# Kernel optimization log

Measured on AMD Instinct MI355X. Metric: run time of the kernel, lower is better.

## Reference

```python
import jax, jax.numpy as jnp
import numpy as np

KERNEL_SIZE = 5
SIGMA = 1.0
DARK_KS = 15


def _gaussian_kernel():
    x = jnp.arange(KERNEL_SIZE, dtype=jnp.float32) - KERNEL_SIZE // 2
    phi = jnp.exp(-0.5 * x * x / (SIGMA ** 2))
    phi = phi / (phi.sum() + 0.001)
    k2d = jnp.outer(phi, phi)                       # [5,5]
    return jnp.tile(k2d[None, None], (3, 1, 1, 1))  # [3,1,5,5] OIHW depthwise


def _tanh01(v):
    return jnp.tanh(v) * 0.5 + 0.5


def setup_inputs() -> dict:
    key = jax.random.key(0)
    k1, k2, k3 = jax.random.split(key, 3)
    # keep x strictly positive so x**param has well-defined gradients
    x = jax.random.uniform(k1, (16, 3, 512, 512), dtype=jnp.float32, minval=0.01, maxval=1.0)
    output1 = jax.random.normal(k2, (16, 7), dtype=jnp.float32)
    output2 = jax.random.normal(k3, (16, 4), dtype=jnp.float32)
    return {"x": x, "output1": output1, "output2": output2}


def reference(x, output1, output2):
    N, C, H, W = x.shape

    # ---- parameter squashing (clip_range + softmax weights) ----
    o1 = jnp.concatenate([
        _tanh01(output1[:, 0:1]) * 0.25 + 1.0,   # gamma param in [1, 1.25]
        _tanh01(output1[:, 1:2]) * 0.9 + 0.1,    # contrast alpha (dead branch)
        _tanh01(output1[:, 2:3]) * 2.0,          # sharpen lamda in [0, 2]
        _tanh01(output1[:, 3:4]),                # dehaze w in [0, 1]
        _tanh01(output1[:, 4:7]) * 0.1 + 0.95,   # WB gains in [0.95, 1.05]
    ], axis=1)
    o2 = jax.nn.softmax(_tanh01(output2), axis=1)  # [N,4] branch weights

    param = o1[:, 0][:, None, None, None]
    lamda = o1[:, 2][:, None, None, None]
    w = o1[:, 3][:, None, None, None]
    wb_params = o1[:, 4:7][:, :, None, None]

    # ---- WB ----
    x1 = jnp.clip(x * wb_params, 0.0, 1.0)

    # ---- GAMMA ----
    x2 = jnp.clip(x ** param + 0.001, 0.0, 1.0)

    # ---- SHARPEN (depthwise 5x5 gaussian blur, unsharp mask) ----
    gk = _gaussian_kernel()
    blur = jax.lax.conv_general_dilated(
        x, gk, window_strides=(1, 1), padding=((2, 2), (2, 2)),
        feature_group_count=3,
        dimension_numbers=("NCHW", "OIHW", "NCHW"))
    blur = jnp.clip(blur, 0.0, 1.0)
    x4 = jnp.clip(x + lamda * (x - blur), 0.0, 1.0)

    # ---- DEHAZE ----
    minc = jnp.min(x, axis=1, keepdims=True)  # [N,1,H,W]
    # avg_pool2d k=15 s=1 p=7 with count_include_pad=True -> sum window / 225
    dark = jax.lax.reduce_window(
        minc, 0.0, jax.lax.add, (1, 1, DARK_KS, DARK_KS), (1, 1, 1, 1),
        padding=[(0, 0), (0, 0), (DARK_KS // 2, DARK_KS // 2), (DARK_KS // 2, DARK_KS // 2)]
    ) / float(DARK_KS * DARK_KS)
    top_k = int(H * W * 0.05)
    flat_dark = dark.reshape(N, -1)
    _, top_idx = jax.lax.top_k(flat_dark, top_k)            # [N, top_k]
    flat_img = x.reshape(N, C, -1)
    sel = jnp.take_along_axis(flat_img, top_idx[:, None, :], axis=2)  # [N,C,top_k]
    A = sel.mean(axis=2)[:, :, None, None]                  # atmospheric light
    trans = 1.0 - w * dark
    trans = jnp.where(trans > 0.1, trans, jnp.float32(0.1))
    x5 = jnp.clip((x - A) / (trans + 0.001) + A, 0.0, 1.0)

    # ---- weighted combination (contrast branch is computed but unused upstream) ----
    w0 = o2[:, 0][:, None, None, None]
    w1 = o2[:, 1][:, None, None, None]
    w2 = o2[:, 2][:, None, None, None]
    w3 = o2[:, 3][:, None, None, None]
    x_sum = x + 0.1 * (w0 * x1 + w1 * x2 + w2 * x4 + w3 * x5)
    x_sum = x_sum / (jnp.sum(o2, axis=1)[:, None, None, None] + 0.001)

    # ---- per-sample per-channel min-max normalization ----
    min_vals = jnp.min(x_sum, axis=(2, 3), keepdims=True)
    max_vals = jnp.max(x_sum, axis=(2, 3), keepdims=True)
    return (x_sum - min_vals) / (max_vals - min_vals + 1e-07)
```

## Files before the change

### kernel.cpp

```cpp
#include <hip/hip_runtime.h>
#include <math.h>

#define NS   16
#define HH   512
#define WW   512
#define HW   (HH*WW)
#define TOPK 13107
#define NBIN 1024

#define O_O1   0
#define O_O2   112
#define O_DEN  176
#define O_KN   304
#define O_MMP  512
#define O_PART 25088
#define O_DARK 33280


#define G0 0.054466787f
#define G1 0.244103071f
#define G2 0.402457854f

__device__ __forceinline__ float tanh01(float v) { return tanhf(v)*0.5f + 0.5f; }
__device__ __forceinline__ float clamp01(float v) { return fminf(fmaxf(v, 0.0f), 1.0f); }
__device__ __forceinline__ int dark_bin(float v) {
  int b = (int)(v * (float)NBIN);
  return b > (NBIN-1) ? (NBIN-1) : (b < 0 ? 0 : b);
}

__device__ __forceinline__ float4 ld_halo(const float* __restrict__ xc, int i,
                                          int h0, int w0, bool interior) {
  int rr = i / 18, q = i - rr*18;
  int gh = h0 - 2 + rr, gw = w0 - 4 + 4*q;
  if (interior) return *(const float4*)&xc[(size_t)gh*WW + gw];
  float4 v; v.x = 0.f; v.y = 0.f; v.z = 0.f; v.w = 0.f;
  if (gh >= 0 && gh < HH && gw >= 0 && gw < WW)
    v = *(const float4*)&xc[(size_t)gh*WW + gw];
  return v;
}

__global__ void __launch_bounds__(512)
k_dark(const float* __restrict__ x, float* __restrict__ wsf, unsigned* __restrict__ hist,
       const float* __restrict__ o1, const float* __restrict__ o2) {
  __shared__ __align__(16) float sm[6240 + 78*64];
  float* minc = sm;
  unsigned* lh = (unsigned*)sm;
  float* hsum = sm + 6240;
  int tid = threadIdx.x;
  int swz = (blockIdx.x & 7) * 128 + (blockIdx.x >> 3);
  int n = swz >> 6, rem = swz & 63;
  int w0 = (rem & 7) * 64, h0 = (rem >> 3) * 64;
  const float* xb = x + (size_t)n*3*HW;

  if (rem == 0 && tid == 0) {
    wsf[O_O1+n*7+0] = tanh01(o1[n*7+0])*0.25f + 1.0f;
    wsf[O_O1+n*7+1] = tanh01(o1[n*7+1])*0.9f  + 0.1f;
    wsf[O_O1+n*7+2] = tanh01(o1[n*7+2])*2.0f;
    wsf[O_O1+n*7+3] = tanh01(o1[n*7+3]);
    wsf[O_O1+n*7+4] = tanh01(o1[n*7+4])*0.1f + 0.95f;
    wsf[O_O1+n*7+5] = tanh01(o1[n*7+5])*0.1f + 0.95f;
    wsf[O_O1+n*7+6] = tanh01(o1[n*7+6])*0.1f + 0.95f;
    float q0 = expf(tanh01(o2[n*4+0]));
    float q1 = expf(tanh01(o2[n*4+1]));
    float q2 = expf(tanh01(o2[n*4+2]));
    float q3 = expf(tanh01(o2[n*4+3]));
    float s = q0+q1+q2+q3;
    q0 /= s; q1 /= s; q2 /= s; q3 /= s;
    wsf[O_O2+n*4+0]=q0; wsf[O_O2+n*4+1]=q1; wsf[O_O2+n*4+2]=q2; wsf[O_O2+n*4+3]=q3;
    wsf[O_DEN+n] = (q0+q1+q2+q3) + 0.001f;
  }

  bool interior = (w0 >= 8) && (w0 + 72 <= WW) && (h0 >= 7) && (h0 + 71 <= HH);
  if (interior) {
    for (int i = tid; i < 78*20; i += 512) {
      int r = i / 20, q = i - r*20;
      size_t o = (size_t)(h0 - 7 + r)*WW + (w0 - 8 + 4*q);
      float4 a = *(const float4*)&xb[o];
      float4 b = *(const float4*)&xb[HW + o];
      float4 c = *(const float4*)&xb[2*HW + o];
      float4 v;
      v.x = fminf(fminf(a.x,b.x),c.x); v.y = fminf(fminf(a.y,b.y),c.y);
      v.z = fminf(fminf(a.z,b.z),c.z); v.w = fminf(fminf(a.w,b.w),c.w);
      *(float4*)&minc[r*80 + 4*q] = v;
    }
  } else {
    for (int i = tid; i < 78*20; i += 512) {
      int r = i / 20, q = i - r*20;
      int hm = h0 - 7 + r, wc = w0 - 8 + 4*q;
      float4 v; v.x = 0.f; v.y = 0.f; v.z = 0.f; v.w = 0.f;
      if (hm >= 0 && hm < HH && wc >= 0 && wc < WW) {
        size_t o = (size_t)hm*WW + wc;
        float4 a = *(const float4*)&xb[o];
        float4 b = *(const float4*)&xb[HW + o];
        float4 c = *(const float4*)&xb[2*HW + o];
        v.x = fminf(fminf(a.x,b.x),c.x); v.y = fminf(fminf(a.y,b.y),c.y);
        v.z = fminf(fminf(a.z,b.z),c.z); v.w = fminf(fminf(a.w,b.w),c.w);
      }
      *(float4*)&minc[r*80 + 4*q] = v;
    }
  }
  __syncthreads();
  for (int i = tid; i < 78*16; i += 512) {
    int r = i >> 4, c4 = (i & 15) * 4;
    const float4* mr = (const float4*)&minc[r*80];
    int qb = c4 >> 2;
    float m[20];
    #pragma unroll
    for (int t = 0; t < 5; ++t) {
      float4 v = mr[qb + t];
      m[4*t] = v.x; m[4*t+1] = v.y; m[4*t+2] = v.z; m[4*t+3] = v.w;
    }
    float s = 0.f;
    #pragma unroll
    for (int j = 1; j <= 15; ++j) s += m[j];
    float4 o;
    o.x = s; s += m[16] - m[1];
    o.y = s; s += m[17] - m[2];
    o.z = s; s += m[18] - m[3];
    o.w = s;
    *(float4*)&hsum[r*64 + c4] = o;
  }
  __syncthreads();
  {
    uint4 z4; z4.x = 0u; z4.y = 0u; z4.z = 0u; z4.w = 0u;
    for (int i = tid; i < NBIN; i += 512) ((uint4*)lh)[i] = z4;
  }
  __syncthreads();
  {
    int c = tid & 63, ty = tid >> 6, r0 = ty * 8;
    int rep = tid & 3;
    float s = 0.f;
    #pragma unroll
    for (int j = 0; j < 15; ++j) s += hsum[(r0 + j)*64 + c];
    float* dk = wsf + O_DARK + (size_t)n*HW;
    int prevb = -1; unsigned cnt = 0;
    #pragma unroll
    for (int i = 0; i < 8; ++i) {
      int r = r0 + i;
      float v = s * (1.0f/225.0f);
      dk[(size_t)(h0 + r)*WW + w0 + c] = v;
      int b = dark_bin(v);
      if (b == prevb) { cnt++; }
      else {
        if (cnt) atomicAdd(&lh[(prevb << 2) | rep], cnt);
        prevb = b; cnt = 1u;
      }
      if (i < 7) s += hsum[(r + 15)*64 + c] - hsum[r*64 + c];
    }
    atomicAdd(&lh[(prevb << 2) | rep], cnt);
  }
  __syncthreads();
  unsigned* gh = hist + n*NBIN;
  for (int b = tid; b < NBIN; b += 512) {
    unsigned v = lh[4*b] + lh[4*b+1] + lh[4*b+2] + lh[4*b+3];
    if (v) atomicAdd(&gh[b], v);
  }
}

__global__ void __launch_bounds__(256)
k_asum(const float* __restrict__ x, float* __restrict__ wsf,
       const unsigned* __restrict__ hist, unsigned* __restrict__ wsu) {
  __shared__ __align__(16) unsigned lh[NBIN];
  __shared__ unsigned spp[256];
  __shared__ unsigned wtot[4];
  __shared__ int sh_bsel;
  __shared__ unsigned sh_kn;
  __shared__ float bl[4][7];
  int tid = threadIdx.x;
  int lane = tid & 63, wave = tid >> 6;
  int swz = (blockIdx.x & 7) * 64 + (blockIdx.x >> 3);
  int n = swz >> 5, chunk = swz & 31;
  {
    uint4 v = ((const uint4*)(hist + n*NBIN))[tid];
    *(uint4*)&lh[tid*4] = v;
    spp[tid] = v.x + v.y + v.z + v.w;
  }
  __syncthreads();
  unsigned sv = spp[tid];
  #pragma unroll
  for (int off = 1; off < 64; off <<= 1) {
    unsigned u = __shfl_down(sv, off);
    if (lane + off < 64) sv += u;
  }
  if (lane == 0) wtot[wave] = sv;
  __syncthreads();
  unsigned above = 0;
  #pragma unroll
  for (int w2 = 1; w2 < 4; ++w2) above += (wave + w2 < 4) ? wtot[wave + w2] : 0u;
  unsigned S = sv + above;
  unsigned Snext = S - spp[tid];
  if (S >= (unsigned)TOPK && Snext < (unsigned)TOPK) {
    unsigned cum = Snext;
    int bsel = tid*4;
    for (int b = tid*4 + 3; b >= tid*4; --b) {
      if (cum + lh[b] >= (unsigned)TOPK) { bsel = b; break; }
      cum += lh[b];
    }
    sh_bsel = bsel;
    sh_kn = (unsigned)TOPK - cum;
  }
  __syncthreads();
  int bsel = sh_bsel;
  if (tid == 0 && chunk == 0) wsu[O_KN + n] = sh_kn;
  const float4* db = (const float4*)(wsf + O_DARK + (size_t)n*HW) + (size_t)chunk*2048;
  const float4* x0 = (const float4*)(x + (size_t)n*3*HW) + (size_t)chunk*2048;
  const float4* x1 = x0 + HW/4;
  const float4* x2 = x0 + HW/2;
  float s0=0,s1=0,s2=0,e0=0,e1=0,e2=0,ec=0;
  #pragma unroll
  for (int k = 0; k < 8; ++k) {
    int idx = k*256 + tid;
    float4 d = db[idx];
    int bbx = dark_bin(d.x), bby = dark_bin(d.y);
    int bbz = dark_bin(d.z), bbw = dark_bin(d.w);
    int bmax = bbx > bby ? bbx : bby;
    bmax = bbz > bmax ? bbz : bmax;
    bmax = bbw > bmax ? bbw : bmax;
    if (bmax >= bsel) {
      float4 a = x0[idx], b = x1[idx], c = x2[idx];
      #define ACC(BB, AX, BX, CX) { \
        bool gt = (BB > bsel), eq = (BB == bsel); \
        s0 += gt ? AX : 0.f; s1 += gt ? BX : 0.f; s2 += gt ? CX : 0.f; \
        e0 += eq ? AX : 0.f; e1 += eq ? BX : 0.f; e2 += eq ? CX : 0.f; \
        ec += eq ? 1.f : 0.f; }
      ACC(bbx, a.x, b.x, c.x) ACC(bby, a.y, b.y, c.y)
      ACC(bbz, a.z, b.z, c.z) ACC(bbw, a.w, b.w, c.w)
      #undef ACC
    }
  }
  #pragma unroll
  for (int off = 32; off; off >>= 1) {
    s0 += __shfl_down(s0, off); s1 += __shfl_down(s1, off); s2 += __shfl_down(s2, off);
    e0 += __shfl_down(e0, off); e1 += __shfl_down(e1, off); e2 += __shfl_down(e2, off);
    ec += __shfl_down(ec, off);
  }
  if (lane == 0) {
    bl[wave][0]=s0; bl[wave][1]=s1; bl[wave][2]=s2;
    bl[wave][3]=e0; bl[wave][4]=e1; bl[wave][5]=e2; bl[wave][6]=ec;
  }
  __syncthreads();
  if (tid < 7) wsf[O_PART + (size_t)swz*8 + tid] =
      bl[0][tid] + bl[1][tid] + bl[2][tid] + bl[3][tid];
}

__global__ void __launch_bounds__(256)
k_main(const float* __restrict__ x, float* __restrict__ wsf,
       const unsigned* __restrict__ wsu, float* __restrict__ out) {
  __shared__ __align__(16) float xs[36*72];
  __shared__ __align__(16) float hb[36*68];
  __shared__ float rmn[4], rmx[4];
  __shared__ float shA[3];
  int tid = threadIdx.x;
  int swz = (blockIdx.x & 7) * 256 + (blockIdx.x >> 3);
  int n = swz >> 7, bxy = swz & 127;
  int w0 = (bxy & 7) * 64, h0 = (bxy >> 3) * 32;
  int r2 = tid >> 4, c4 = (tid & 15) * 4;
  int wave = tid >> 6, lane = tid & 63;
  const float* dkp = wsf + O_DARK + (size_t)n*HW + (size_t)(h0 + 2*r2)*WW + w0 + c4;
  float4 dk0 = *(const float4*)dkp;
  float4 dk1 = *(const float4*)(dkp + WW);
  float param = wsf[O_O1 + n*7 + 0];
  float lamda = wsf[O_O1 + n*7 + 2];
  float wpar  = wsf[O_O1 + n*7 + 3];
  float wbc[3];
  wbc[0] = wsf[O_O1 + n*7 + 4];
  wbc[1] = wsf[O_O1 + n*7 + 5];
  wbc[2] = wsf[O_O1 + n*7 + 6];
  float q0 = wsf[O_O2 + n*4 + 0], q1 = wsf[O_O2 + n*4 + 1];
  float q2 = wsf[O_O2 + n*4 + 2], q3 = wsf[O_O2 + n*4 + 3];
  float rden = 1.0f / wsf[O_DEN + n];
  bool interior = (w0 >= 4) && (w0 + 68 <= WW) && (h0 >= 2) && (h0 + 34 <= HH);
  if (tid < 64) {
    float s0=0,s1=0,s2=0,e0=0,e1=0,e2=0,ec=0;
    if (tid < 32) {
      const float* p = wsf + O_PART + (size_t)(n*32 + tid)*8;
      s0=p[0]; s1=p[1]; s2=p[2]; e0=p[3]; e1=p[4]; e2=p[5]; ec=p[6];
    }
    #pragma unroll
    for (int off = 32; off; off >>= 1) {
      s0 += __shfl_down(s0, off); s1 += __shfl_down(s1, off); s2 += __shfl_down(s2, off);
      e0 += __shfl_down(e0, off); e1 += __shfl_down(e1, off); e2 += __shfl_down(e2, off);
      ec += __shfl_down(ec, off);
    }
    if (tid == 0) {
      float kn = (float)wsu[O_KN + n];
      float ce = fmaxf(ec, 1.0f);
      shA[0] = (s0 + kn * (e0 / ce)) * (1.0f/(float)TOPK);
      shA[1] = (s1 + kn * (e1 / ce)) * (1.0f/(float)TOPK);
      shA[2] = (s2 + kn * (e2 / ce)) * (1.0f/(float)TOPK);
    }
  }

  float4 pf0, pf1, pf2;
  #define LOADCH(cc) do { \
    const float* xc = x + (size_t)(n*3 + (cc))*HW; \
    pf0 = ld_halo(xc, tid,       h0, w0, interior); \
    pf1 = ld_halo(xc, tid + 256, h0, w0, interior); \
    if (tid < 136) pf2 = ld_halo(xc, tid + 512, h0, w0, interior); \
  } while (0)
  #define STORECH() do { \
    { int rr = tid/18, q = tid - rr*18; *(float4*)&xs[rr*72 + 4*q] = pf0; } \
    { int i2 = tid + 256; int rr = i2/18, q = i2 - rr*18; *(float4*)&xs[rr*72 + 4*q] = pf1; } \
    if (tid < 136) { int i2 = tid + 512; int rr = i2/18, q = i2 - rr*18; *(float4*)&xs[rr*72 + 4*q] = pf2; } \
  } while (0)

  LOADCH(0);
  STORECH();
  __syncthreads();

  for (int c = 0; c < 3; ++c) {
    int z = n*3 + c;
    for (int i = tid; i < 576; i += 256) {
      int rr = i >> 4, cc4 = (i & 15) * 4;
      const float4* xr = (const float4*)&xs[rr*72];
      int qb = cc4 >> 2;
      float4 A4 = xr[qb], B4 = xr[qb+1], C4 = xr[qb+2];
      float m2=A4.z, m3=A4.w, m4=B4.x, m5=B4.y, m6=B4.z, m7=B4.w, m8=C4.x, m9=C4.y;
      float4 o;
      o.x = G0*(m2+m6) + G1*(m3+m5) + G2*m4;
      o.y = G0*(m3+m7) + G1*(m4+m6) + G2*m5;
      o.z = G0*(m4+m8) + G1*(m5+m7) + G2*m6;
      o.w = G0*(m5+m9) + G1*(m6+m8) + G2*m7;
      *(float4*)&hb[rr*68 + cc4] = o;
    }
    if (c < 2) LOADCH(c + 1);
    __syncthreads();
    float wb = wbc[c];
    float A  = shA[c];
    float4 xv0 = *(const float4*)&xs[(2*r2+2)*72 + c4 + 4];
    float4 xv1 = *(const float4*)&xs[(2*r2+3)*72 + c4 + 4];
    float4 b0 = *(const float4*)&hb[(2*r2+0)*68 + c4];
    float4 b1 = *(const float4*)&hb[(2*r2+1)*68 + c4];
    float4 b2 = *(const float4*)&hb[(2*r2+2)*68 + c4];
    float4 b3 = *(const float4*)&hb[(2*r2+3)*68 + c4];
    float4 b4 = *(const float4*)&hb[(2*r2+4)*68 + c4];
    float4 b5 = *(const float4*)&hb[(2*r2+5)*68 + c4];
    float4 os0, os1;
    float mnv = 3.4e38f, mxv = -3.4e38f;
    #define PIX(OX, XV, B0, B1, B2, B3, B4, DK) { \
      float blur = clamp01(G0*(B0+B4) + G1*(B1+B3) + G2*B2); \
      float x4v = clamp01(XV + lamda*(XV - blur)); \
      float x1v = clamp01(XV * wb); \
      float x2v = clamp01(__expf(param*__logf(XV)) + 0.001f); \
      float tr = 1.0f - wpar*DK; tr = tr > 0.1f ? tr : 0.1f; \
      float x5v = clamp01((XV - A) * __builtin_amdgcn_rcpf(tr + 0.001f) + A); \
      OX = (XV + 0.1f*(q0*x1v + q1*x2v + q2*x4v + q3*x5v)) * rden; \
      mnv = fminf(mnv, OX); mxv = fmaxf(mxv, OX); }
    PIX(os0.x, xv0.x, b0.x, b1.x, b2.x, b3.x, b4.x, dk0.x)
    PIX(os0.y, xv0.y, b0.y, b1.y, b2.y, b3.y, b4.y, dk0.y)
    PIX(os0.z, xv0.z, b0.z, b1.z, b2.z, b3.z, b4.z, dk0.z)
    PIX(os0.w, xv0.w, b0.w, b1.w, b2.w, b3.w, b4.w, dk0.w)
    PIX(os1.x, xv1.x, b1.x, b2.x, b3.x, b4.x, b5.x, dk1.x)
    PIX(os1.y, xv1.y, b1.y, b2.y, b3.y, b4.y, b5.y, dk1.y)
    PIX(os1.z, xv1.z, b1.z, b2.z, b3.z, b4.z, b5.z, dk1.z)
    PIX(os1.w, xv1.w, b1.w, b2.w, b3.w, b4.w, b5.w, dk1.w)
    #undef PIX
    float* op = out + (size_t)z*HW + (size_t)(h0 + 2*r2)*WW + w0 + c4;
    *(float4*)op = os0;
    *(float4*)(op + WW) = os1;
    #pragma unroll
    for (int off = 32; off; off >>= 1) {
      mnv = fminf(mnv, __shfl_down(mnv, off));
      mxv = fmaxf(mxv, __shfl_down(mxv, off));
    }
    if (lane == 0) { rmn[wave] = mnv; rmx[wave] = mxv; }
    __syncthreads();
    if (tid == 0) {
      mnv = fminf(fminf(rmn[0], rmn[1]), fminf(rmn[2], rmn[3]));
      mxv = fmaxf(fmaxf(rmx[0], rmx[1]), fmaxf(rmx[2], rmx[3]));
      wsf[O_MMP + z*512 + bxy]       = mnv;
      wsf[O_MMP + z*512 + 256 + bxy] = mxv;
    }
    if (c < 2) {
      STORECH();
      __syncthreads();
    }
  }
  #undef LOADCH
  #undef STORECH
}

__global__ void __launch_bounds__(256)
k_norm(float* __restrict__ out, const float* __restrict__ wsf) {
  int tid = threadIdx.x;
  int bid = (blockIdx.x & 7) * 192 + (blockIdx.x >> 3);
  int nc = bid >> 5;
  int sub = bid & 31;
  int l = tid & 63;
  const float* pm = wsf + O_MMP + (size_t)nc*512;
  float mn = fminf(pm[l], pm[64 + l]);
  float mx = fmaxf(pm[256 + l], pm[320 + l]);
  #pragma unroll
  for (int off = 32; off; off >>= 1) {
    mn = fminf(mn, __shfl_down(mn, off));
    mx = fmaxf(mx, __shfl_down(mx, off));
  }
  mn = __shfl(mn, 0);
  mx = __shfl(mx, 0);
  float sc = 1.0f / (mx - mn + 1e-7f);
  float4* o4 = (float4*)out + (size_t)nc*65536 + (size_t)sub*2048;
  #pragma unroll
  for (int k = 0; k < 8; ++k) {
    float4 v = o4[k*256 + tid];
    v.x = (v.x - mn) * sc; v.y = (v.y - mn) * sc;
    v.z = (v.z - mn) * sc; v.w = (v.w - mn) * sc;
    o4[k*256 + tid] = v;
  }
}

extern "C" void kernel_launch(void* const* d_in, const int* in_sizes, int n_in,
                              void* d_out, int out_size, void* d_ws, size_t ws_size,
                              hipStream_t stream) {
  const float* x  = (const float*)d_in[0];
  const float* o1 = (const float*)d_in[1];
  const float* o2 = (const float*)d_in[2];
  float* out = (float*)d_out;
  float* wsf = (float*)d_ws;
  unsigned* wsu = (unsigned*)d_ws;
  unsigned* hist = (unsigned*)(out + (size_t)16*HW);

  hipMemsetAsync(hist, 0, (size_t)NS*NBIN*sizeof(unsigned), stream);
  k_dark<<<dim3(1024), dim3(512), 0, stream>>>(x, wsf, hist, o1, o2);
  k_asum<<<dim3(512), dim3(256), 0, stream>>>(x, wsf, hist, wsu);
  k_main<<<dim3(2048), dim3(256), 0, stream>>>(x, wsf, wsu, out);
  k_norm<<<dim3(1536), dim3(256), 0, stream>>>(out, wsf);
}
```

Baseline: 154.3 us.

## Fuse horizontal and vertical blur passes in registers, dropping shared blur buffer

Replaces the two-phase separable blur, which wrote horizontal results to a shared buffer and synchronized before the vertical pass, with per-thread computation. Each thread computes the six horizontal rows it needs and accumulates the vertical taps directly in registers. This removes the hb shared array and one __syncthreads per channel, and pads the xs row stride from 72 to 76 floats, likely to reduce LDS bank conflicts. In exchange each thread recomputes horizontal rows that neighbours also compute, adding redundant ALU work and LDS reads.

```diff
diff --git a/kernel.cpp b/kernel.cpp
--- a/kernel.cpp
+++ b/kernel.cpp
@@ -246,8 +246,7 @@
 __global__ void __launch_bounds__(256)
 k_main(const float* __restrict__ x, float* __restrict__ wsf,
        const unsigned* __restrict__ wsu, float* __restrict__ out) {
-  __shared__ __align__(16) float xs[36*72];
-  __shared__ __align__(16) float hb[36*68];
+  __shared__ __align__(16) float xs[36*76];
   __shared__ float rmn[4], rmx[4];
   __shared__ float shA[3];
   int tid = threadIdx.x;
@@ -299,46 +298,46 @@
     if (tid < 136) pf2 = ld_halo(xc, tid + 512, h0, w0, interior); \
   } while (0)
   #define STORECH() do { \
-    { int rr = tid/18, q = tid - rr*18; *(float4*)&xs[rr*72 + 4*q] = pf0; } \
-    { int i2 = tid + 256; int rr = i2/18, q = i2 - rr*18; *(float4*)&xs[rr*72 + 4*q] = pf1; } \
-    if (tid < 136) { int i2 = tid + 512; int rr = i2/18, q = i2 - rr*18; *(float4*)&xs[rr*72 + 4*q] = pf2; } \
+    { int rr = tid/18, q = tid - rr*18; *(float4*)&xs[rr*76 + 4*q] = pf0; } \
+    { int i2 = tid + 256; int rr = i2/18, q = i2 - rr*18; *(float4*)&xs[rr*76 + 4*q] = pf1; } \
+    if (tid < 136) { int i2 = tid + 512; int rr = i2/18, q = i2 - rr*18; *(float4*)&xs[rr*76 + 4*q] = pf2; } \
   } while (0)
 
   LOADCH(0);
   STORECH();
   __syncthreads();
 
+  int qb = c4 >> 2;
   for (int c = 0; c < 3; ++c) {
     int z = n*3 + c;
-    for (int i = tid; i < 576; i += 256) {
-      int rr = i >> 4, cc4 = (i & 15) * 4;
-      const float4* xr = (const float4*)&xs[rr*72];
-      int qb = cc4 >> 2;
+    if (c < 2) LOADCH(c + 1);
+    float4 acc0, acc1;
+    acc0.x = acc0.y = acc0.z = acc0.w = 0.f;
+    acc1.x = acc1.y = acc1.z = acc1.w = 0.f;
+    const float cA[6] = {G0, G1, G2, G1, G0, 0.f};
+    const float cB[6] = {0.f, G0, G1, G2, G1, G0};
+    #pragma unroll
+    for (int k = 0; k < 6; ++k) {
+      const float4* xr = (const float4*)&xs[(2*r2 + k)*76];
       float4 A4 = xr[qb], B4 = xr[qb+1], C4 = xr[qb+2];
       float m2=A4.z, m3=A4.w, m4=B4.x, m5=B4.y, m6=B4.z, m7=B4.w, m8=C4.x, m9=C4.y;
-      float4 o;
-      o.x = G0*(m2+m6) + G1*(m3+m5) + G2*m4;
-      o.y = G0*(m3+m7) + G1*(m4+m6) + G2*m5;
-      o.z = G0*(m4+m8) + G1*(m5+m7) + G2*m6;
-      o.w = G0*(m5+m9) + G1*(m6+m8) + G2*m7;
-      *(float4*)&hb[rr*68 + cc4] = o;
-    }
-    if (c < 2) LOADCH(c + 1);
-    __syncthreads();
+      float4 h;
+      h.x = G0*(m2+m6) + G1*(m3+m5) + G2*m4;
+      h.y = G0*(m3+m7) + G1*(m4+m6) + G2*m5;
+      h.z = G0*(m4+m8) + G1*(m5+m7) + G2*m6;
+      h.w = G0*(m5+m9) + G1*(m6+m8) + G2*m7;
+      float wa = cA[k], wb2 = cB[k];
+      acc0.x += wa*h.x; acc0.y += wa*h.y; acc0.z += wa*h.z; acc0.w += wa*h.w;
+      acc1.x += wb2*h.x; acc1.y += wb2*h.y; acc1.z += wb2*h.z; acc1.w += wb2*h.w;
+    }
     float wb = wbc[c];
     float A  = shA[c];
-    float4 xv0 = *(const float4*)&xs[(2*r2+2)*72 + c4 + 4];
-    float4 xv1 = *(const float4*)&xs[(2*r2+3)*72 + c4 + 4];
-    float4 b0 = *(const float4*)&hb[(2*r2+0)*68 + c4];
-    float4 b1 = *(const float4*)&hb[(2*r2+1)*68 + c4];
-    float4 b2 = *(const float4*)&hb[(2*r2+2)*68 + c4];
-    float4 b3 = *(const float4*)&hb[(2*r2+3)*68 + c4];
-    float4 b4 = *(const float4*)&hb[(2*r2+4)*68 + c4];
-    float4 b5 = *(const float4*)&hb[(2*r2+5)*68 + c4];
+    float4 xv0 = *(const float4*)&xs[(2*r2+2)*76 + c4 + 4];
+    float4 xv1 = *(const float4*)&xs[(2*r2+3)*76 + c4 + 4];
     float4 os0, os1;
     float mnv = 3.4e38f, mxv = -3.4e38f;
-    #define PIX(OX, XV, B0, B1, B2, B3, B4, DK) { \
-      float blur = clamp01(G0*(B0+B4) + G1*(B1+B3) + G2*B2); \
+    #define PIX(OX, XV, BL, DK) { \
+      float blur = clamp01(BL); \
       float x4v = clamp01(XV + lamda*(XV - blur)); \
       float x1v = clamp01(XV * wb); \
       float x2v = clamp01(__expf(param*__logf(XV)) + 0.001f); \
@@ -346,14 +345,14 @@
       float x5v = clamp01((XV - A) * __builtin_amdgcn_rcpf(tr + 0.001f) + A); \
       OX = (XV + 0.1f*(q0*x1v + q1*x2v + q2*x4v + q3*x5v)) * rden; \
       mnv = fminf(mnv, OX); mxv = fmaxf(mxv, OX); }
-    PIX(os0.x, xv0.x, b0.x, b1.x, b2.x, b3.x, b4.x, dk0.x)
-    PIX(os0.y, xv0.y, b0.y, b1.y, b2.y, b3.y, b4.y, dk0.y)
-    PIX(os0.z, xv0.z, b0.z, b1.z, b2.z, b3.z, b4.z, dk0.z)
-    PIX(os0.w, xv0.w, b0.w, b1.w, b2.w, b3.w, b4.w, dk0.w)
-    PIX(os1.x, xv1.x, b1.x, b2.x, b3.x, b4.x, b5.x, dk1.x)
-    PIX(os1.y, xv1.y, b1.y, b2.y, b3.y, b4.y, b5.y, dk1.y)
-    PIX(os1.z, xv1.z, b1.z, b2.z, b3.z, b4.z, b5.z, dk1.z)
-    PIX(os1.w, xv1.w, b1.w, b2.w, b3.w, b4.w, b5.w, dk1.w)
+    PIX(os0.x, xv0.x, acc0.x, dk0.x)
+    PIX(os0.y, xv0.y, acc0.y, dk0.y)
+    PIX(os0.z, xv0.z, acc0.z, dk0.z)
+    PIX(os0.w, xv0.w, acc0.w, dk0.w)
+    PIX(os1.x, xv1.x, acc1.x, dk1.x)
+    PIX(os1.y, xv1.y, acc1.y, dk1.y)
+    PIX(os1.z, xv1.z, acc1.z, dk1.z)
+    PIX(os1.w, xv1.w, acc1.w, dk1.w)
     #undef PIX
     float* op = out + (size_t)z*HW + (size_t)(h0 + 2*r2)*WW + w0 + c4;
     *(float4*)op = os0;
```

Result: slower. 162.7 us (+5.5%).
